# Kernel tuning notes

Measured on AMD Instinct MI355X. Metric: run time of the kernel, lower is better.

## Reference

```python
import jax, jax.numpy as jnp
import numpy as np

NC = 80            # number of classes (COCO)
NM = 32            # mask coefficients (YOLOv5-seg)
D = 4 + 1 + NC + NM
N_ANCHORS = 100800  # 1280x1280 input, strides 8/16/32, 3 anchors
CONF_THRES = 0.25
IOU_THRES = 0.45
MAX_DET = 300
TOPK = 4096        # fixed pre-NMS candidate budget (jit-compatible stand-in for boolean filter)


def setup_inputs() -> dict:
    key = jax.random.key(0)
    x = jax.random.uniform(key, (1, N_ANCHORS, D), dtype=jnp.float32)
    return {"x": x}


def _pairwise_iou(boxes):
    # boxes: [K, 4] in (y1, x1, y2, x2)
    y1, x1, y2, x2 = boxes[:, 0], boxes[:, 1], boxes[:, 2], boxes[:, 3]
    area = (y2 - y1) * (x2 - x1)
    iy1 = jnp.maximum(y1[:, None], y1[None, :])
    ix1 = jnp.maximum(x1[:, None], x1[None, :])
    iy2 = jnp.minimum(y2[:, None], y2[None, :])
    ix2 = jnp.minimum(x2[:, None], x2[None, :])
    inter = jnp.clip(iy2 - iy1, 0.0) * jnp.clip(ix2 - ix1, 0.0)
    union = area[:, None] + area[None, :] - inter
    return inter / jnp.maximum(union, 1e-9)


def reference(x):
    p = x[0]                                   # [N, D] (loop returns after first image)
    obj = p[:, 4]
    valid = obj > CONF_THRES                   # candidates = obj score > conf_thres
    cls_scores = p[:, 5:5 + NC] * obj[:, None] # scores = cls * obj
    scores = jnp.max(cls_scores, axis=1)
    classes = jnp.argmax(cls_scores, axis=1).astype(x.dtype)
    # xywh (center) -> yxyx
    xc, yc, w, h = p[:, 0], p[:, 1], p[:, 2], p[:, 3]
    yxyx = jnp.stack([yc - h * 0.5, xc - w * 0.5, yc + h * 0.5, xc + w * 0.5], axis=1)
    masks = p[:, 5 + NC:]                      # [N, NM]
    # replace torch's boolean-filter gather with fixed-size top-K over masked scores
    scores_m = jnp.where(valid, scores, -1.0)
    top_s, top_i = jax.lax.top_k(scores_m, TOPK)   # sorted desc, as torchvision nms requires
    b = yxyx[top_i]                            # [K, 4]
    keep0 = top_s > -0.5                       # only real candidates
    iou = _pairwise_iou(b)                     # [K, K]
    j_idx = jnp.arange(TOPK)

    def body(i, keep):
        sup = keep[i] & (iou[i] > IOU_THRES) & (j_idx > i)
        return keep & ~sup

    keep = jax.lax.fori_loop(0, TOPK, body, keep0)
    # pad/select top MAX_DET surviving detections (score -1.0 marks padding)
    sel_s = jnp.where(keep, top_s, -1.0)
    out_s, out_i = jax.lax.top_k(sel_s, MAX_DET)
    gi = top_i[out_i]
    return (yxyx[gi][None], classes[gi][None], out_s[None], masks[gi][None])
```

## Files before the change

kernel.cpp:

```cpp
#include <hip/hip_runtime.h>


#define AS1 __attribute__((address_space(1)))
#define AS3 __attribute__((address_space(3)))

constexpr int    N_ANCH = 100800;
constexpr int    DIMV   = 117;
constexpr int    TOPKN  = 4096;
constexpr int    MAXDET = 300;
constexpr int    KCAP   = 12288;
constexpr int    NBUCK  = 16384;
constexpr int    NSLICE = 16;

constexpr int PACK_TOT = 133120;

constexpr size_t WS_HIST   = 0;
constexpr size_t WS_SLICES = WS_HIST   + 65536;
constexpr size_t WS_SCORES = WS_SLICES + (size_t)NSLICE * NBUCK * 4;
constexpr size_t WS_CLS    = WS_SCORES + (size_t)N_ANCH * 4;
constexpr size_t WS_SEL    = WS_CLS    + (size_t)N_ANCH * 4;
constexpr size_t WS_KEYS   = WS_SEL    + 256;
constexpr size_t WS_RANK   = WS_KEYS   + (size_t)KCAP * 8;
constexpr size_t WS_SIDX   = WS_RANK   + (size_t)KCAP * 4;
constexpr size_t WS_SSC    = WS_SIDX   + 4096ull * 4;
constexpr size_t WS_BOXES  = WS_SSC    + 4096ull * 4;
constexpr size_t WS_MASKP  = WS_BOXES  + 4096ull * 16;
constexpr size_t WS_DIAG   = WS_MASKP  + (size_t)PACK_TOT * 8 + 4096;
constexpr size_t WS_OUTI   = WS_DIAG   + 4096ull * 8;
constexpr size_t WS_OUTS   = WS_OUTI   + 1280;

__global__ void zero_kernel(unsigned* __restrict__ slices, int* __restrict__ sel) {
    int i = blockIdx.x * 256 + threadIdx.x;
    if (i < NSLICE * NBUCK) slices[i] = 0u;
    if (i < 64)             sel[i]    = 0;
}

constexpr int SROWS = 64;
__global__ void score_kernel(const float* __restrict__ x, float* __restrict__ scores,
                             int* __restrict__ cls, unsigned* __restrict__ slices) {
    __shared__ float sx[SROWS * DIMV];
    int block0 = blockIdx.x * SROWS;
    const float4* src = (const float4*)(x + (size_t)block0 * DIMV);
    float4* dst = (float4*)sx;
    constexpr int NV4 = SROWS * DIMV / 4;
    for (int i = threadIdx.x; i < NV4; i += 128) dst[i] = src[i];
    __syncthreads();
    int row  = threadIdx.x >> 1;
    int half = threadIdx.x & 1;
    const float* rp = sx + row * DIMV;
    float obj = rp[4];
    const float* cp = rp + 5 + half * 40;
    float best = -1.0f;
    int   bc   = half * 40;
#pragma unroll 8
    for (int c = 0; c < 40; ++c) {
        float s = __fmul_rn(cp[c], obj);
        if (s > best) { best = s; bc = half * 40 + c; }
    }
    float so = __shfl_xor(best, 1);
    int   co = __shfl_xor(bc, 1);
    if (half == 0) {
        if (so > best) { best = so; bc = co; }
        int a = block0 + row;
        bool valid = obj > 0.25f;
        scores[a] = valid ? best : -1.0f;
        cls[a]    = bc;
        if (valid) {
            unsigned b = __float_as_uint(best) >> 16;
            atomicAdd(&slices[(blockIdx.x & (NSLICE - 1)) * NBUCK + b], 1u);
        }
    }
}

__global__ void reduce_hist_kernel(const unsigned* __restrict__ slices,
                                   unsigned* __restrict__ hist) {
    int b = blockIdx.x * 256 + threadIdx.x;
    unsigned s = 0;
#pragma unroll
    for (int k = 0; k < NSLICE; ++k) s += slices[(size_t)k * NBUCK + b];
    hist[b] = s;
}

__global__ void select_kernel(const unsigned* __restrict__ hist, int* sel) {
    __shared__ unsigned sv[1024];
    int t = threadIdx.x;
    int base = NBUCK - 16 * (t + 1);
    const uint4* hp = (const uint4*)(hist + base);
    unsigned hb[16];
    unsigned own = 0;
#pragma unroll
    for (int q = 0; q < 4; ++q) {
        uint4 v = hp[q];
        hb[q * 4 + 0] = v.x; hb[q * 4 + 1] = v.y;
        hb[q * 4 + 2] = v.z; hb[q * 4 + 3] = v.w;
        own += v.x + v.y + v.z + v.w;
    }
    sv[t] = own;
    __syncthreads();
    for (int off = 1; off < 1024; off <<= 1) {
        unsigned v = (t >= off) ? sv[t - off] : 0u;
        __syncthreads();
        sv[t] += v;
        __syncthreads();
    }
    unsigned incl = sv[t];
    unsigned before = incl - own;
    if (before < (unsigned)TOPKN && incl >= (unsigned)TOPKN) {
        unsigned running = before;
        for (int k = 15; k >= 0; --k) {
            running += hb[k];
            if (running >= (unsigned)TOPKN) {
                sel[0] = base + k;
                sel[1] = (int)(running - hb[k]);
                break;
            }
        }
    }
}

__global__ void compact_kernel(const float* __restrict__ scores, int* sel,
                               unsigned long long* __restrict__ keys,
                               int* __restrict__ rank) {
    int a = blockIdx.x * blockDim.x + threadIdx.x;
    if (a < KCAP) rank[a] = 0;
    if (a >= N_ANCH) return;
    float s = scores[a];
    if (s < 0.0f) return;
    unsigned bits = __float_as_uint(s);
    if ((int)(bits >> 16) < sel[0]) return;
    int pos = atomicAdd(&sel[2], 1);
    if (pos < KCAP) keys[pos] = ((unsigned long long)bits << 32) | (unsigned)(~a);
}

constexpr int NCOLP = 8;
__global__ void rank_kernel(const unsigned long long* __restrict__ keys,
                            const int* __restrict__ sel, int* __restrict__ rank) {
    __shared__ unsigned long long tile[2048];
    int n = sel[2]; if (n > KCAP) n = KCAP;
    if (blockIdx.x * 256 >= n) return;
    int t0 = blockIdx.y * 2048;
    if (t0 >= n) return;
    int i = blockIdx.x * 256 + threadIdx.x;
    unsigned long long myKey = (i < n) ? keys[i] : 0ull;
    int m = n - t0; if (m > 2048) m = 2048;
    for (int j = threadIdx.x; j < m; j += 256) tile[j] = keys[t0 + j];
    __syncthreads();
    int cnt = 0;
    int j = 0;
    for (; j + 3 < m; j += 4) {
        cnt += (tile[j]     > myKey);
        cnt += (tile[j + 1] > myKey);
        cnt += (tile[j + 2] > myKey);
        cnt += (tile[j + 3] > myKey);
    }
    for (; j < m; ++j) cnt += (tile[j] > myKey);
    if (i < n && cnt) atomicAdd(&rank[i], cnt);
}

__global__ void scatter_kernel(const float* __restrict__ x,
                               const unsigned long long* __restrict__ keys,
                               const int* __restrict__ sel, const int* __restrict__ rank,
                               int* __restrict__ sidx, float* __restrict__ sscore,
                               float* __restrict__ boxes) {
    int n = sel[2]; if (n > KCAP) n = KCAP;
    int i = blockIdx.x * 256 + threadIdx.x;
    if (i >= n) return;
    int r = rank[i];
    if (r >= TOPKN) return;
    unsigned long long k = keys[i];
    int a = (int)(~(unsigned)(k & 0xFFFFFFFFull));
    sidx[r]   = a;
    sscore[r] = __uint_as_float((unsigned)(k >> 32));
    const float* p = x + (size_t)a * DIMV;
    float xc = p[0], yc = p[1], w = p[2], h = p[3];
    float hw = __fmul_rn(w, 0.5f);
    float hh = __fmul_rn(h, 0.5f);
    boxes[r * 4 + 0] = __fsub_rn(yc, hh);
    boxes[r * 4 + 1] = __fsub_rn(xc, hw);
    boxes[r * 4 + 2] = __fadd_rn(yc, hh);
    boxes[r * 4 + 3] = __fadd_rn(xc, hw);
}

__global__ void iou_mask_kernel(const float* __restrict__ boxes,
                                unsigned long long* __restrict__ maskp,
                                unsigned long long* __restrict__ diag) {
    int colT = blockIdx.x, rowT = blockIdx.y;
    if (colT < rowT) return;
    int t = threadIdx.x;
    __shared__ float cb[64][5];
    const float4* bp = (const float4*)boxes;
    int cj = colT * 64 + t;
    {
        float4 c = bp[cj];
        cb[t][0] = c.x; cb[t][1] = c.y; cb[t][2] = c.z; cb[t][3] = c.w;
        cb[t][4] = __fmul_rn(__fsub_rn(c.z, c.x), __fsub_rn(c.w, c.y));
    }
    __syncthreads();
    int r = rowT * 64 + t;
    float4 rv = bp[r];
    float ry1 = rv.x, rx1 = rv.y, ry2 = rv.z, rx2 = rv.w;
    float rarea = __fmul_rn(__fsub_rn(ry2, ry1), __fsub_rn(rx2, rx1));
    unsigned long long bitsw = 0ull;
#pragma unroll 8
    for (int j = 0; j < 64; ++j) {
        float iy1 = fmaxf(ry1, cb[j][0]);
        float ix1 = fmaxf(rx1, cb[j][1]);
        float iy2 = fminf(ry2, cb[j][2]);
        float ix2 = fminf(rx2, cb[j][3]);
        float ih = fmaxf(__fsub_rn(iy2, iy1), 0.0f);
        float iw = fmaxf(__fsub_rn(ix2, ix1), 0.0f);
        float inter = __fmul_rn(ih, iw);
        float uni = __fsub_rn(__fadd_rn(rarea, cb[j][4]), inter);
        float iou = __fdiv_rn(inter, fmaxf(uni, 1e-9f));
        if (iou > 0.45f && (colT * 64 + j) > r) bitsw |= (1ull << j);
    }
    int pb = 64 * (64 * rowT - (rowT * (rowT - 1)) / 2);
    maskp[pb + t * (64 - rowT) + (colT - rowT)] = bitsw;
    if (colT == rowT) diag[(rowT << 6) + t] = bitsw;
}

__device__ __forceinline__ unsigned long long readlane64(unsigned long long v, int l) {
    unsigned lo = (unsigned)__builtin_amdgcn_readlane((int)(unsigned)(v & 0xFFFFFFFFull), l);
    unsigned hi = (unsigned)__builtin_amdgcn_readlane((int)(unsigned)(v >> 32), l);
    return ((unsigned long long)hi << 32) | lo;
}

__global__ void __launch_bounds__(64, 1)
nms_scan_kernel(const unsigned long long* __restrict__ maskp,
                const unsigned long long* __restrict__ diagG,
                const float* __restrict__ sscore,
                int* __restrict__ outIdx, float* __restrict__ outScore) {
    int lane = threadIdx.x;
    unsigned long long remv = 0ull;
    __shared__ __align__(16) unsigned long long ldsAll[20224];
    constexpr int slotW[4] = {0, 4096, 8192, 12160};
    unsigned long long* diagLds = ldsAll + 16128;
    int count = 0;

    auto issueBatch = [&](int w) {
        if (w >= 64) return;
        int L = (65 - w) >> 1;
        const char* gbase = (const char*)maskp +
                            (size_t)(64 * (64 * w - (w * (w - 1)) / 2)) * 8 +
                            (size_t)lane * 16;
        char* lbase = (char*)(ldsAll + slotW[w & 3]);
        for (int i = 0; i < L; ++i) {
            __builtin_amdgcn_global_load_lds(
                (AS1 const unsigned*)(gbase + (size_t)i * 1024),
                (AS3 unsigned*)(lbase + (size_t)i * 1024), 16, 0, 0);
        }
    };

    {
        const char* gb = (const char*)diagG + (size_t)lane * 16;
        char* lb = (char*)diagLds;
#pragma unroll
        for (int i = 0; i < 32; ++i) {
            __builtin_amdgcn_global_load_lds(
                (AS1 const unsigned*)(gb + (size_t)i * 1024),
                (AS3 unsigned*)(lb + (size_t)i * 1024), 16, 0, 0);
        }
    }
    issueBatch(0); issueBatch(1); issueBatch(2);

#define VW(n) asm volatile("s_waitcnt vmcnt(" #n ")" ::: "memory")

    for (int w = 0; w < 64 && count < MAXDET; ++w) {
        issueBatch(w + 3);
        unsigned long long cand = ~readlane64(remv, w);
        if (!cand) continue;
        int P = ((w + 1 < 64) ? ((64 - w) >> 1) : 0)
              + ((w + 2 < 64) ? ((63 - w) >> 1) : 0)
              + ((w + 3 < 64) ? ((62 - w) >> 1) : 0);
        if (P < 63) {
            switch (P >> 1) {
                case  0: VW(0);  break; case  1: VW(2);  break;
                case  2: VW(4);  break; case  3: VW(6);  break;
                case  4: VW(8);  break; case  5: VW(10); break;
                case  6: VW(12); break; case  7: VW(14); break;
                case  8: VW(16); break; case  9: VW(18); break;
                case 10: VW(20); break; case 11: VW(22); break;
                case 12: VW(24); break; case 13: VW(26); break;
                case 14: VW(28); break; case 15: VW(30); break;
                case 16: VW(32); break; case 17: VW(34); break;
                case 18: VW(36); break; case 19: VW(38); break;
                case 20: VW(40); break; case 21: VW(42); break;
                case 22: VW(44); break; case 23: VW(46); break;
                case 24: VW(48); break; case 25: VW(50); break;
                case 26: VW(52); break; case 27: VW(54); break;
                case 28: VW(56); break; case 29: VW(58); break;
                case 30: VW(60); break; default: VW(62); break;
            }
        } else {
            asm volatile("" ::: "memory");
        }
        const unsigned long long* trow = ldsAll + slotW[w & 3];
        int stride = 64 - w;
        unsigned long long diagv = diagLds[(w << 6) | lane];
        unsigned long long alive = cand;
        unsigned long long keptM = 0ull;
        int* keepArr = (int*)diagLds;
        while (alive && count < MAXDET) {
            int b = (int)__builtin_ctzll(alive);
            unsigned long long db = readlane64(diagv, b);
            if (lane == 0) keepArr[count] = (w << 6) + b;
            count++;
            keptM |= (1ull << b);
            alive &= ~(db | (1ull << b));
        }
        int rel = lane - w;
        while (keptM) {
            int bs[4]; unsigned long long t2 = keptM; int g = 0;
#pragma unroll
            for (int t = 0; t < 4; ++t) {
                bs[t] = t2 ? (int)__builtin_ctzll(t2) : 0;
                if (t2) { t2 &= t2 - 1; g = t + 1; }
            }
            unsigned long long vs[4];
#pragma unroll
            for (int t = 0; t < 4; ++t)
                vs[t] = (rel >= 0) ? trow[bs[t] * stride + rel] : 0ull;
#pragma unroll
            for (int t = 0; t < 4; ++t)
                if (t < g) remv |= vs[t];
            keptM = t2;
        }
    }
    __syncthreads();
    unsigned long long* remvFinal = ldsAll;
    remvFinal[lane] = remv;
    __syncthreads();
    int K = count;
    int* keepArr = (int*)diagLds;
    for (int k = lane; k < K; k += 64) {
        int s = keepArr[k];
        outIdx[k] = s;
        outScore[k] = sscore[s];
    }
    if (K < MAXDET && lane == 0) {
        int filled = K;
        for (int w = 0; w < 64 && filled < MAXDET; ++w) {
            unsigned long long word = remvFinal[w];
            while (word && filled < MAXDET) {
                int b = (int)__builtin_ctzll(word);
                word &= word - 1;
                outIdx[filled] = (w << 6) + b;
                outScore[filled] = -1.0f;
                filled++;
            }
        }
    }
}

__global__ void write_out_kernel(const float* __restrict__ x, const int* __restrict__ sidx,
                                 const int* __restrict__ cls, const float* __restrict__ boxes,
                                 const int* __restrict__ outIdx, const float* __restrict__ outScore,
                                 float* __restrict__ out) {
    int o = blockIdx.x;
    int t = threadIdx.x;
    int s = outIdx[o];
    int a = sidx[s];
    if (t < 32) {
        out[1800 + o * 32 + t] = x[(size_t)a * DIMV + 85 + t];
    } else if (t < 36) {
        out[o * 4 + (t - 32)] = boxes[s * 4 + (t - 32)];
    } else if (t == 36) {
        out[1200 + o] = (float)cls[a];
    } else if (t == 37) {
        out[1500 + o] = outScore[o];
    }
}

extern "C" void kernel_launch(void* const* d_in, const int* in_sizes, int n_in,
                              void* d_out, int out_size, void* d_ws, size_t ws_size,
                              hipStream_t stream) {
    const float* x = (const float*)d_in[0];
    char* ws = (char*)d_ws;
    unsigned*            hist   = (unsigned*)(ws + WS_HIST);
    unsigned*            slices = (unsigned*)(ws + WS_SLICES);
    float*               scores = (float*)(ws + WS_SCORES);
    int*                 cls    = (int*)(ws + WS_CLS);
    int*                 sel    = (int*)(ws + WS_SEL);
    unsigned long long*  keys   = (unsigned long long*)(ws + WS_KEYS);
    int*                 rank   = (int*)(ws + WS_RANK);
    int*                 sidx   = (int*)(ws + WS_SIDX);
    float*               sscore = (float*)(ws + WS_SSC);
    float*               boxes  = (float*)(ws + WS_BOXES);
    unsigned long long*  maskp  = (unsigned long long*)(ws + WS_MASKP);
    unsigned long long*  diag   = (unsigned long long*)(ws + WS_DIAG);
    int*                 outIdx = (int*)(ws + WS_OUTI);
    float*               outSc  = (float*)(ws + WS_OUTS);

    zero_kernel<<<(NSLICE * NBUCK + 255) / 256, 256, 0, stream>>>(slices, sel);
    score_kernel<<<N_ANCH / SROWS, 128, 0, stream>>>(x, scores, cls, slices);
    reduce_hist_kernel<<<NBUCK / 256, 256, 0, stream>>>(slices, hist);
    select_kernel<<<1, 1024, 0, stream>>>(hist, sel);
    compact_kernel<<<(N_ANCH + 255) / 256, 256, 0, stream>>>(scores, sel, keys, rank);
    dim3 rg(KCAP / 256, NCOLP);
    rank_kernel<<<rg, 256, 0, stream>>>(keys, sel, rank);
    scatter_kernel<<<KCAP / 256, 256, 0, stream>>>(x, keys, sel, rank, sidx, sscore, boxes);
    dim3 mg(64, 64);
    iou_mask_kernel<<<mg, 64, 0, stream>>>(boxes, maskp, diag);
    nms_scan_kernel<<<1, 64, 0, stream>>>(maskp, diag, sscore, outIdx, outSc);
    write_out_kernel<<<MAXDET, 64, 0, stream>>>(x, sidx, cls, boxes, outIdx, outSc, (float*)d_out);
}
```

Before: 223.6 us.

## Warp-specialize NMS scan with producer waves and fuse output writing

The single-wave NMS scan kernel becomes a 320-thread block. Wave 0 runs the sequential suppression scan, and four producer waves stream the per-row mask tiles into a 4-slot LDS ring, coordinating through ready/done flags in shared memory instead of vmcnt counting in one wave. The final output gather (boxes, class, score, mask coefficients) is fused into the same kernel, removing the separate write_out launch and the global index/score staging. This adds spin-wait overhead. The fused output loop also writes less coalesced output, with one thread writing 32 mask floats.

```diff
diff --git a/kernel.cpp b/kernel.cpp
--- a/kernel.cpp
+++ b/kernel.cpp
@@ -26,8 +26,6 @@
 constexpr size_t WS_BOXES  = WS_SSC    + 4096ull * 4;
 constexpr size_t WS_MASKP  = WS_BOXES  + 4096ull * 16;
 constexpr size_t WS_DIAG   = WS_MASKP  + (size_t)PACK_TOT * 8 + 4096;
-constexpr size_t WS_OUTI   = WS_DIAG   + 4096ull * 8;
-constexpr size_t WS_OUTS   = WS_OUTI   + 1280;
 
 __global__ void zero_kernel(unsigned* __restrict__ slices, int* __restrict__ sel) {
     int i = blockIdx.x * 256 + threadIdx.x;
@@ -225,149 +223,169 @@
     return ((unsigned long long)hi << 32) | lo;
 }
 
-__global__ void __launch_bounds__(64, 1)
+#define VW0() asm volatile("s_waitcnt vmcnt(0)" ::: "memory")
+
+__global__ void __launch_bounds__(320, 1)
 nms_scan_kernel(const unsigned long long* __restrict__ maskp,
                 const unsigned long long* __restrict__ diagG,
                 const float* __restrict__ sscore,
-                int* __restrict__ outIdx, float* __restrict__ outScore) {
-    int lane = threadIdx.x;
+                const float* __restrict__ x,
+                const int* __restrict__ sidx,
+                const int* __restrict__ cls,
+                const float* __restrict__ boxes,
+                float* __restrict__ out) {
+    __shared__ __align__(16) unsigned long long ldsAll[16128];
+    __shared__ __align__(16) unsigned long long diagLds[4096];
+    __shared__ int ready[64];
+    __shared__ int doneC[64];
+    __shared__ int finiF;
+    __shared__ int KK;
+    constexpr int slotW[4] = {0, 4096, 8192, 12160};
+
+    int wave = threadIdx.x >> 6;
+    int lane = threadIdx.x & 63;
+
+    if (threadIdx.x < 64) { ready[threadIdx.x] = 0; doneC[threadIdx.x] = 0; }
+    if (threadIdx.x == 0) { finiF = 0; KK = 0; }
+    __syncthreads();
+
     unsigned long long remv = 0ull;
-    __shared__ __align__(16) unsigned long long ldsAll[20224];
-    constexpr int slotW[4] = {0, 4096, 8192, 12160};
-    unsigned long long* diagLds = ldsAll + 16128;
     int count = 0;
 
-    auto issueBatch = [&](int w) {
-        if (w >= 64) return;
-        int L = (65 - w) >> 1;
-        const char* gbase = (const char*)maskp +
-                            (size_t)(64 * (64 * w - (w * (w - 1)) / 2)) * 8 +
-                            (size_t)lane * 16;
-        char* lbase = (char*)(ldsAll + slotW[w & 3]);
-        for (int i = 0; i < L; ++i) {
-            __builtin_amdgcn_global_load_lds(
-                (AS1 const unsigned*)(gbase + (size_t)i * 1024),
-                (AS3 unsigned*)(lbase + (size_t)i * 1024), 16, 0, 0);
-        }
-    };
-
-    {
-        const char* gb = (const char*)diagG + (size_t)lane * 16;
-        char* lb = (char*)diagLds;
-#pragma unroll
-        for (int i = 0; i < 32; ++i) {
-            __builtin_amdgcn_global_load_lds(
-                (AS1 const unsigned*)(gb + (size_t)i * 1024),
-                (AS3 unsigned*)(lb + (size_t)i * 1024), 16, 0, 0);
-        }
-    }
-    issueBatch(0); issueBatch(1); issueBatch(2);
-
-#define VW(n) asm volatile("s_waitcnt vmcnt(" #n ")" ::: "memory")
-
-    for (int w = 0; w < 64 && count < MAXDET; ++w) {
-        issueBatch(w + 3);
-        unsigned long long cand = ~readlane64(remv, w);
-        if (!cand) continue;
-        int P = ((w + 1 < 64) ? ((64 - w) >> 1) : 0)
-              + ((w + 2 < 64) ? ((63 - w) >> 1) : 0)
-              + ((w + 3 < 64) ? ((62 - w) >> 1) : 0);
-        if (P < 63) {
-            switch (P >> 1) {
-                case  0: VW(0);  break; case  1: VW(2);  break;
-                case  2: VW(4);  break; case  3: VW(6);  break;
-                case  4: VW(8);  break; case  5: VW(10); break;
-                case  6: VW(12); break; case  7: VW(14); break;
-                case  8: VW(16); break; case  9: VW(18); break;
-                case 10: VW(20); break; case 11: VW(22); break;
-                case 12: VW(24); break; case 13: VW(26); break;
-                case 14: VW(28); break; case 15: VW(30); break;
-                case 16: VW(32); break; case 17: VW(34); break;
-                case 18: VW(36); break; case 19: VW(38); break;
-                case 20: VW(40); break; case 21: VW(42); break;
-                case 22: VW(44); break; case 23: VW(46); break;
-                case 24: VW(48); break; case 25: VW(50); break;
-                case 26: VW(52); break; case 27: VW(54); break;
-                case 28: VW(56); break; case 29: VW(58); break;
-                case 30: VW(60); break; default: VW(62); break;
-            }
-        } else {
+    if (wave == 0) {
+        {
+            const char* gb = (const char*)diagG + (size_t)lane * 16;
+            char* lb = (char*)diagLds;
+#pragma unroll
+            for (int i = 0; i < 32; ++i) {
+                __builtin_amdgcn_global_load_lds(
+                    (AS1 const unsigned*)(gb + (size_t)i * 1024),
+                    (AS3 unsigned*)(lb + (size_t)i * 1024), 16, 0, 0);
+            }
+            VW0();
             asm volatile("" ::: "memory");
         }
-        const unsigned long long* trow = ldsAll + slotW[w & 3];
-        int stride = 64 - w;
-        unsigned long long diagv = diagLds[(w << 6) | lane];
-        unsigned long long alive = cand;
-        unsigned long long keptM = 0ull;
-        int* keepArr = (int*)diagLds;
-        while (alive && count < MAXDET) {
-            int b = (int)__builtin_ctzll(alive);
-            unsigned long long db = readlane64(diagv, b);
-            if (lane == 0) keepArr[count] = (w << 6) + b;
-            count++;
-            keptM |= (1ull << b);
-            alive &= ~(db | (1ull << b));
-        }
-        int rel = lane - w;
-        while (keptM) {
-            int bs[4]; unsigned long long t2 = keptM; int g = 0;
-#pragma unroll
-            for (int t = 0; t < 4; ++t) {
-                bs[t] = t2 ? (int)__builtin_ctzll(t2) : 0;
-                if (t2) { t2 &= t2 - 1; g = t + 1; }
-            }
-            unsigned long long vs[4];
-#pragma unroll
-            for (int t = 0; t < 4; ++t)
-                vs[t] = (rel >= 0) ? trow[bs[t] * stride + rel] : 0ull;
-#pragma unroll
-            for (int t = 0; t < 4; ++t)
-                if (t < g) remv |= vs[t];
-            keptM = t2;
-        }
-    }
-    __syncthreads();
-    unsigned long long* remvFinal = ldsAll;
-    remvFinal[lane] = remv;
-    __syncthreads();
-    int K = count;
-    int* keepArr = (int*)diagLds;
-    for (int k = lane; k < K; k += 64) {
-        int s = keepArr[k];
-        outIdx[k] = s;
-        outScore[k] = sscore[s];
-    }
-    if (K < MAXDET && lane == 0) {
+        int* keepArrL = (int*)diagLds;
+        for (int w = 0; w < 64 && count < MAXDET; ++w) {
+            unsigned long long cand = ~readlane64(remv, w);
+            if (!cand) {
+                if (lane == 0) doneC[w] = 1;
+                continue;
+            }
+            unsigned long long diagv = diagLds[(w << 6) | lane];
+            {
+                volatile int* rf = &ready[w];
+                while (*rf == 0) {}
+            }
+            asm volatile("" ::: "memory");
+            const unsigned long long* trow = ldsAll + slotW[w & 3];
+            int stride = 64 - w;
+            unsigned long long alive = cand;
+            unsigned long long keptM = 0ull;
+            while (alive && count < MAXDET) {
+                int b = (int)__builtin_ctzll(alive);
+                unsigned long long db = readlane64(diagv, b);
+                if (lane == 0) keepArrL[count] = (w << 6) + b;
+                count++;
+                keptM |= (1ull << b);
+                alive &= ~(db | (1ull << b));
+            }
+            int rel = lane - w;
+            while (keptM) {
+                int bs[8]; unsigned long long t2 = keptM; int g = 0;
+#pragma unroll
+                for (int t = 0; t < 8; ++t) {
+                    bs[t] = t2 ? (int)__builtin_ctzll(t2) : 0;
+                    if (t2) { t2 &= t2 - 1; g = t + 1; }
+                }
+                unsigned long long vs[8];
+#pragma unroll
+                for (int t = 0; t < 8; ++t)
+                    vs[t] = (rel >= 0) ? trow[bs[t] * stride + rel] : 0ull;
+#pragma unroll
+                for (int t = 0; t < 8; ++t)
+                    if (t < g) remv |= vs[t];
+                keptM = t2;
+            }
+            asm volatile("" ::: "memory");
+            if (lane == 0) doneC[w] = 1;
+        }
+        asm volatile("" ::: "memory");
+        if (lane == 0) finiF = 1;
+    } else {
+        int p = wave - 1;
+        for (int w = p; w < 64; w += 4) {
+            if (w >= 4) {
+                volatile int* dc = &doneC[w - 4];
+                volatile int* ff = &finiF;
+                bool fin = false;
+                for (;;) {
+                    if (*dc) break;
+                    if (*ff) { fin = true; break; }
+                }
+                if (fin) break;
+            }
+            int L = (65 - w) >> 1;
+            const char* gbase = (const char*)maskp +
+                                (size_t)(64 * (64 * w - (w * (w - 1)) / 2)) * 8 +
+                                (size_t)lane * 16;
+            char* lbase = (char*)(ldsAll + slotW[w & 3]);
+            for (int i = 0; i < L; ++i) {
+                __builtin_amdgcn_global_load_lds(
+                    (AS1 const unsigned*)(gbase + (size_t)i * 1024),
+                    (AS3 unsigned*)(lbase + (size_t)i * 1024), 16, 0, 0);
+            }
+            VW0();
+            asm volatile("" ::: "memory");
+            if (lane == 0) ready[w] = 1;
+        }
+    }
+
+    __syncthreads();
+
+    unsigned long long* remvF = ldsAll;
+    if (wave == 0) {
+        remvF[lane] = remv;
+        if (lane == 0) KK = count;
+    }
+    __syncthreads();
+
+    int K = KK;
+    int* keepArrL = (int*)diagLds;
+    int* sArr     = (int*)diagLds + 384;
+    float* scArr  = (float*)diagLds + 768;
+    for (int o = threadIdx.x; o < K; o += 320) {
+        int s = keepArrL[o];
+        sArr[o]  = s;
+        scArr[o] = sscore[s];
+    }
+    if (threadIdx.x == 0 && K < MAXDET) {
         int filled = K;
-        for (int w = 0; w < 64 && filled < MAXDET; ++w) {
-            unsigned long long word = remvFinal[w];
+        for (int w2 = 0; w2 < 64 && filled < MAXDET; ++w2) {
+            unsigned long long word = remvF[w2];
             while (word && filled < MAXDET) {
                 int b = (int)__builtin_ctzll(word);
                 word &= word - 1;
-                outIdx[filled] = (w << 6) + b;
-                outScore[filled] = -1.0f;
+                sArr[filled]  = (w2 << 6) + b;
+                scArr[filled] = -1.0f;
                 filled++;
             }
         }
     }
-}
-
-__global__ void write_out_kernel(const float* __restrict__ x, const int* __restrict__ sidx,
-                                 const int* __restrict__ cls, const float* __restrict__ boxes,
-                                 const int* __restrict__ outIdx, const float* __restrict__ outScore,
-                                 float* __restrict__ out) {
-    int o = blockIdx.x;
-    int t = threadIdx.x;
-    int s = outIdx[o];
-    int a = sidx[s];
-    if (t < 32) {
-        out[1800 + o * 32 + t] = x[(size_t)a * DIMV + 85 + t];
-    } else if (t < 36) {
-        out[o * 4 + (t - 32)] = boxes[s * 4 + (t - 32)];
-    } else if (t == 36) {
+    __syncthreads();
+
+    for (int o = threadIdx.x; o < MAXDET; o += 320) {
+        int s = sArr[o];
+        int a = sidx[s];
+        out[o * 4 + 0] = boxes[s * 4 + 0];
+        out[o * 4 + 1] = boxes[s * 4 + 1];
+        out[o * 4 + 2] = boxes[s * 4 + 2];
+        out[o * 4 + 3] = boxes[s * 4 + 3];
         out[1200 + o] = (float)cls[a];
-    } else if (t == 37) {
-        out[1500 + o] = outScore[o];
+        out[1500 + o] = scArr[o];
+        const float* mp = x + (size_t)a * DIMV + 85;
+#pragma unroll
+        for (int k = 0; k < 32; ++k) out[1800 + o * 32 + k] = mp[k];
     }
 }
 
@@ -388,8 +406,6 @@
     float*               boxes  = (float*)(ws + WS_BOXES);
     unsigned long long*  maskp  = (unsigned long long*)(ws + WS_MASKP);
     unsigned long long*  diag   = (unsigned long long*)(ws + WS_DIAG);
-    int*                 outIdx = (int*)(ws + WS_OUTI);
-    float*               outSc  = (float*)(ws + WS_OUTS);
 
     zero_kernel<<<(NSLICE * NBUCK + 255) / 256, 256, 0, stream>>>(slices, sel);
     score_kernel<<<N_ANCH / SROWS, 128, 0, stream>>>(x, scores, cls, slices);
@@ -401,6 +417,6 @@
     scatter_kernel<<<KCAP / 256, 256, 0, stream>>>(x, keys, sel, rank, sidx, sscore, boxes);
     dim3 mg(64, 64);
     iou_mask_kernel<<<mg, 64, 0, stream>>>(boxes, maskp, diag);
-    nms_scan_kernel<<<1, 64, 0, stream>>>(maskp, diag, sscore, outIdx, outSc);
-    write_out_kernel<<<MAXDET, 64, 0, stream>>>(x, sidx, cls, boxes, outIdx, outSc, (float*)d_out);
-}
+    nms_scan_kernel<<<1, 320, 0, stream>>>(maskp, diag, sscore, x, sidx, cls, boxes,
+                                           (float*)d_out);
+}
```

After: 220.5 us. About the same (-1.4%).
